# Kernel optimization log

Hardware: AMD Instinct MI355X
Metric: run time of the kernel (lower is better)

## Reference

```python
import jax, jax.numpy as jnp
import numpy as np

B, C, H, W = 8, 64, 256, 256   # input images
FH, FW = 64, 64                # low-res feature map
S = 256                        # superpixels per image (num[i] == S)


def setup_inputs() -> dict:
    key = jax.random.key(0)
    k1, k2, k3 = jax.random.split(key, 3)
    inp = jax.random.normal(k1, (B, C, H, W), dtype=jnp.float32)
    feat = jax.random.normal(k2, (B, C, FH, FW), dtype=jnp.float32)
    sp = jax.random.randint(k3, (B, 1, H, W), 0, S).astype(jnp.int64)
    num = jnp.full((B,), S, dtype=jnp.int64)
    return {"input": inp, "feature": feat, "sp": sp, "num": num}


def bilinear_align_corners(x, out_h, out_w):
    # F.interpolate(x, size, mode='bilinear', align_corners=True)
    _, _, in_h, in_w = x.shape
    ys = jnp.linspace(0.0, in_h - 1.0, out_h)
    xs = jnp.linspace(0.0, in_w - 1.0, out_w)
    y0 = jnp.floor(ys).astype(jnp.int32)
    x0 = jnp.floor(xs).astype(jnp.int32)
    y1 = jnp.minimum(y0 + 1, in_h - 1)
    x1 = jnp.minimum(x0 + 1, in_w - 1)
    wy = (ys - y0.astype(ys.dtype)).reshape(1, 1, out_h, 1)
    wx = (xs - x0.astype(xs.dtype)).reshape(1, 1, 1, out_w)
    rows = x[:, :, y0, :] * (1.0 - wy) + x[:, :, y1, :] * wy   # [B,C,out_h,in_w]
    return rows[:, :, :, x0] * (1.0 - wx) + rows[:, :, :, x1] * wx


def segment_scalar_means(x, sp, num):
    # torch: mean_values[i][j] = mean(x[i][sp[i]==j]) over channels AND pixels
    b = x.shape[0]
    px = x.mean(axis=1).reshape(b, -1)           # channel-mean per pixel [B, HW]
    ids = sp.reshape(b, -1)                      # [B, HW]
    seg_sum = jax.vmap(lambda v, i: jax.ops.segment_sum(v, i, num_segments=S))(px, ids)
    seg_cnt = jax.vmap(lambda i: jax.ops.segment_sum(jnp.ones(i.shape, jnp.float32), i, num_segments=S))(ids)
    m = jnp.where(seg_cnt > 0, seg_sum / jnp.maximum(seg_cnt, 1.0), 0.0)  # nan_to_num(0)
    valid = jnp.arange(S)[None, :] < num[:, None]                          # j < num[i]
    return jnp.where(valid, m, 0.0)              # [B, S]


def similarity_matrix(m):
    # mean_values broadcast to [B,S,C] => 1 - ||diff||/sqrt(C) == 1 - |m_j - m_k|
    return 1.0 - jnp.abs(m[:, :, None] - m[:, None, :])   # [B, S, S]


def reference(input, feature, sp, num):
    feat = bilinear_align_corners(feature, input.shape[-1], input.shape[-1])
    mat1 = similarity_matrix(segment_scalar_means(input, sp, num))
    mat2 = similarity_matrix(segment_scalar_means(feat, sp, num))
    return jnp.mean(jnp.abs(mat1 - mat2))   # nn.L1Loss()
```

## Files before the change

kernel.cpp:

```cpp
#include <hip/hip_runtime.h>

#define NB 8
#define NC 64
#define NH 256
#define NW 256
#define HW (NH*NW)
#define NFH 64
#define NFW 64
#define FHW (NFH*NFW)
#define NS 256
#define PPB 1024
#define NPB (HW/PPB)
#define NG 4
#define CPG (NC/NG)
#define NMAIN (NB*NPB*NG)
#define NRB (NB*NPB)

__global__ __launch_bounds__(256) void fmean_k(const float* __restrict__ feature,
                                               float* __restrict__ fmean) {
  __shared__ float4 s_p[8][32];
  const int b     = blockIdx.x >> 5;
  const int chunk = blockIdx.x & 31;
  const int q  = threadIdx.x & 31;
  const int cg = threadIdx.x >> 5;

  const float4* src = reinterpret_cast<const float4*>(
      feature + (size_t)(b * NC + cg * 8) * FHW) + chunk * 32 + q;
  float4 a = make_float4(0.f, 0.f, 0.f, 0.f);
  #pragma unroll
  for (int c = 0; c < 8; ++c) {
    float4 v = src[(size_t)c * (FHW / 4)];
    a.x += v.x; a.y += v.y; a.z += v.z; a.w += v.w;
  }
  s_p[cg][q] = a;
  __syncthreads();
  if (threadIdx.x < 32) {
    float4 r = make_float4(0.f, 0.f, 0.f, 0.f);
    #pragma unroll
    for (int g = 0; g < 8; ++g) {
      float4 v = s_p[g][threadIdx.x];
      r.x += v.x; r.y += v.y; r.z += v.z; r.w += v.w;
    }
    const float s = 1.0f / NC;
    r.x *= s; r.y *= s; r.z *= s; r.w *= s;
    reinterpret_cast<float4*>(fmean + (size_t)b * FHW)[chunk * 32 + threadIdx.x] = r;
  }
}

__global__ __launch_bounds__(256) void
main_k(const float* __restrict__ input,
       const int* __restrict__ sp,
       const float* __restrict__ fmean,
       float* __restrict__ part1,
       float* __restrict__ part2,
       float* __restrict__ partc,
       unsigned* __restrict__ counter) {
  __shared__ float s_f[FHW];
  __shared__ float s_bins[NS];
  __shared__ float s_fb[NS];
  __shared__ unsigned s_cnt[NS];

  const int bid = blockIdx.x;
  const int tid = threadIdx.x;
  if (bid == 0 && tid == 0) *counter = 0u;

  const int g  = bid & (NG - 1);
  const int pb = (bid >> 2) & (NPB - 1);
  const int b  = bid >> 8;
  const bool roleB = (g == 0);

  s_bins[tid] = 0.f;
  if (roleB) {
    const float4* fsrc = reinterpret_cast<const float4*>(fmean + (size_t)b * FHW);
    #pragma unroll
    for (int i = 0; i < 4; ++i)
      reinterpret_cast<float4*>(s_f)[tid + 256 * i] = fsrc[tid + 256 * i];
    s_fb[tid] = 0.f;
    s_cnt[tid] = 0u;
  }
  __syncthreads();

  const int p0 = pb * PPB + tid * 4;
  const float* ib = input + (size_t)(b * NC + g * CPG) * HW + p0;
  float4 acc = make_float4(0.f, 0.f, 0.f, 0.f);
  #pragma unroll 8
  for (int c = 0; c < CPG; ++c) {
    float4 v = *reinterpret_cast<const float4*>(ib + (size_t)c * HW);
    acc.x += v.x; acc.y += v.y; acc.z += v.z; acc.w += v.w;
  }
  const int4 idv = *reinterpret_cast<const int4*>(sp + (size_t)b * HW + p0);
  const float s = 1.0f / NC;
  atomicAdd(&s_bins[idv.x], acc.x * s);
  atomicAdd(&s_bins[idv.y], acc.y * s);
  atomicAdd(&s_bins[idv.z], acc.z * s);
  atomicAdd(&s_bins[idv.w], acc.w * s);

  if (roleB) {
    const int ids[4] = {idv.x, idv.y, idv.z, idv.w};
    const int h = p0 >> 8;
    const float yd = (float)h * (63.0f / 255.0f);
    const int y0 = (int)yd;
    const float wy = yd - (float)y0;
    const int y1 = min(y0 + 1, NFH - 1);
    const float* row0 = s_f + y0 * NFW;
    const float* row1 = s_f + y1 * NFW;
    #pragma unroll
    for (int i = 0; i < 4; ++i) {
      const int w = (p0 & 255) + i;
      const float xd = (float)w * (63.0f / 255.0f);
      const int x0 = (int)xd;
      const float wx = xd - (float)x0;
      const int x1 = min(x0 + 1, NFW - 1);
      float v0 = row0[x0] * (1.f - wy) + row1[x0] * wy;
      float v1 = row0[x1] * (1.f - wy) + row1[x1] * wy;
      float fv = v0 * (1.f - wx) + v1 * wx;
      atomicAdd(&s_fb[ids[i]], fv);
      atomicAdd(&s_cnt[ids[i]], 1u);
    }
  }
  __syncthreads();

  part1[(size_t)bid * NS + tid] = s_bins[tid];
  if (roleB) {
    const int r = (b << 6) | pb;
    part2[(size_t)r * NS + tid] = s_fb[tid];
    partc[(size_t)r * NS + tid] = (float)s_cnt[tid];
  }
}

__global__ __launch_bounds__(256) void
finalize_k(const float* __restrict__ part1,
           const float* __restrict__ part2,
           const float* __restrict__ partc,
           const int* __restrict__ num,
           float* __restrict__ partial,
           unsigned* __restrict__ counter,
           float* __restrict__ out) {
  __shared__ float m1[NS];
  __shared__ float m2[NS];
  __shared__ float red[256];
  const int b = blockIdx.x;
  const int j = threadIdx.x;

  float s1 = 0.f;
  const float* p1 = part1 + (size_t)b * 256 * NS + j;
  #pragma unroll 8
  for (int t = 0; t < 256; ++t) s1 += p1[(size_t)t * NS];

  float s2 = 0.f, c = 0.f;
  const float* p2 = part2 + (size_t)b * 64 * NS + j;
  const float* pc = partc + (size_t)b * 64 * NS + j;
  #pragma unroll 8
  for (int t = 0; t < 64; ++t) { s2 += p2[(size_t)t * NS]; c += pc[(size_t)t * NS]; }

  const int nb = num[b];
  float v1 = 0.f, v2 = 0.f;
  if (j < nb && c > 0.f) {
    float invc = 1.0f / c;
    v1 = s1 * invc;
    v2 = s2 * invc;
  }
  m1[j] = v1; m2[j] = v2;
  __syncthreads();

  float accum = 0.f;
  #pragma unroll 8
  for (int k = 0; k < NS; ++k) {
    accum += fabsf(fabsf(v1 - m1[k]) - fabsf(v2 - m2[k]));
  }
  red[j] = accum;
  __syncthreads();
  for (int st = 128; st > 0; st >>= 1) {
    if (j < st) red[j] += red[j + st];
    __syncthreads();
  }

  if (j == 0) {
    atomicExch(&partial[b], red[0]);
    __threadfence();
    unsigned old = atomicAdd(counter, 1u);
    if (old == NB - 1) {
      __threadfence();
      float sAll = 0.f;
      #pragma unroll
      for (int i = 0; i < NB; ++i) sAll += atomicAdd(&partial[i], 0.0f);
      out[0] = sAll / (float)(NB * NS * NS);
      *counter = 0u;
    }
  }
}

extern "C" void kernel_launch(void* const* d_in, const int* in_sizes, int n_in,
                              void* d_out, int out_size, void* d_ws, size_t ws_size,
                              hipStream_t stream) {
  const float* input   = (const float*)d_in[0];
  const float* feature = (const float*)d_in[1];
  const int*   sp      = (const int*)d_in[2];
  const int*   num     = (const int*)d_in[3];
  float* out = (float*)d_out;

  float* ws      = (float*)d_ws;
  float*    part1   = ws;
  float*    part2   = part1 + (size_t)NMAIN * NS;
  float*    partc   = part2 + (size_t)NRB * NS;
  float*    fmean   = partc + (size_t)NRB * NS;
  float*    partial = fmean + NB * FHW;
  unsigned* counter = (unsigned*)(partial + 8);

  fmean_k<<<NB * 32, 256, 0, stream>>>(feature, fmean);
  main_k<<<NMAIN, 256, 0, stream>>>(input, sp, fmean, part1, part2, partc, counter);
  finalize_k<<<NB, 256, 0, stream>>>(part1, part2, partc, num, partial, counter, out);
}
```

Baseline: 63.02 us.

## Split feature-bilinear work into separate blocks and drop 16KB shared fmean tile

The bilinear/count work no longer runs inside one of every four input-reduction blocks. It now goes to 512 extra dedicated blocks that read the feature mean directly from global memory instead of staging a 16KB shared tile. This removes the per-block shared-memory footprint and the load imbalance between role-B and regular blocks, which should raise occupancy for the bandwidth-bound input reduction. Input loads also switch to nontemporal vector loads. The cost is that sp is now read twice for the role-B pixels and the fmean reads become uncached gathers from global memory.

```diff
diff --git a/kernel.cpp b/kernel.cpp
--- a/kernel.cpp
+++ b/kernel.cpp
@@ -16,6 +16,8 @@
 #define NMAIN (NB*NPB*NG)
 #define NRB (NB*NPB)
 
+typedef float f32x4 __attribute__((ext_vector_type(4)));
+
 __global__ __launch_bounds__(256) void fmean_k(const float* __restrict__ feature,
                                                float* __restrict__ fmean) {
   __shared__ float4 s_p[8][32];
@@ -55,7 +57,6 @@
        float* __restrict__ part2,
        float* __restrict__ partc,
        unsigned* __restrict__ counter) {
-  __shared__ float s_f[FHW];
   __shared__ float s_bins[NS];
   __shared__ float s_fb[NS];
   __shared__ unsigned s_cnt[NS];
@@ -64,46 +65,54 @@
   const int tid = threadIdx.x;
   if (bid == 0 && tid == 0) *counter = 0u;
 
-  const int g  = bid & (NG - 1);
-  const int pb = (bid >> 2) & (NPB - 1);
-  const int b  = bid >> 8;
-  const bool roleB = (g == 0);
-
-  s_bins[tid] = 0.f;
-  if (roleB) {
-    const float4* fsrc = reinterpret_cast<const float4*>(fmean + (size_t)b * FHW);
+  if (bid < NMAIN) {
+    const int g  = bid & (NG - 1);
+    const int pb = (bid >> 2) & (NPB - 1);
+    const int b  = bid >> 8;
+
+    s_bins[tid] = 0.f;
+    __syncthreads();
+
+    const int p0 = pb * PPB + tid * 4;
+    const float* ib = input + (size_t)(b * NC + g * CPG) * HW + p0;
+    f32x4 acc = (f32x4)(0.f);
     #pragma unroll
-    for (int i = 0; i < 4; ++i)
-      reinterpret_cast<float4*>(s_f)[tid + 256 * i] = fsrc[tid + 256 * i];
+    for (int c = 0; c < CPG; ++c) {
+      f32x4 v = __builtin_nontemporal_load(
+          reinterpret_cast<const f32x4*>(ib + (size_t)c * HW));
+      acc += v;
+    }
+    const int4 idv = *reinterpret_cast<const int4*>(sp + (size_t)b * HW + p0);
+    const float s = 1.0f / NC;
+    atomicAdd(&s_bins[idv.x], acc.x * s);
+    atomicAdd(&s_bins[idv.y], acc.y * s);
+    atomicAdd(&s_bins[idv.z], acc.z * s);
+    atomicAdd(&s_bins[idv.w], acc.w * s);
+    __syncthreads();
+
+    part1[(size_t)bid * NS + tid] = s_bins[tid];
+  } else {
+    const int r  = bid - NMAIN;
+    const int b  = r >> 6;
+    const int pb = r & (NPB - 1);
+
     s_fb[tid] = 0.f;
     s_cnt[tid] = 0u;
-  }
-  __syncthreads();
-
-  const int p0 = pb * PPB + tid * 4;
-  const float* ib = input + (size_t)(b * NC + g * CPG) * HW + p0;
-  float4 acc = make_float4(0.f, 0.f, 0.f, 0.f);
-  #pragma unroll 8
-  for (int c = 0; c < CPG; ++c) {
-    float4 v = *reinterpret_cast<const float4*>(ib + (size_t)c * HW);
-    acc.x += v.x; acc.y += v.y; acc.z += v.z; acc.w += v.w;
-  }
-  const int4 idv = *reinterpret_cast<const int4*>(sp + (size_t)b * HW + p0);
-  const float s = 1.0f / NC;
-  atomicAdd(&s_bins[idv.x], acc.x * s);
-  atomicAdd(&s_bins[idv.y], acc.y * s);
-  atomicAdd(&s_bins[idv.z], acc.z * s);
-  atomicAdd(&s_bins[idv.w], acc.w * s);
-
-  if (roleB) {
+    __syncthreads();
+
+    const int p0 = pb * PPB + tid * 4;
+    const int4 idv = *reinterpret_cast<const int4*>(sp + (size_t)b * HW + p0);
     const int ids[4] = {idv.x, idv.y, idv.z, idv.w};
+
+    const float* fm = fmean + (size_t)b * FHW;
     const int h = p0 >> 8;
     const float yd = (float)h * (63.0f / 255.0f);
     const int y0 = (int)yd;
     const float wy = yd - (float)y0;
     const int y1 = min(y0 + 1, NFH - 1);
-    const float* row0 = s_f + y0 * NFW;
-    const float* row1 = s_f + y1 * NFW;
+    const float* row0 = fm + y0 * NFW;
+    const float* row1 = fm + y1 * NFW;
+
     #pragma unroll
     for (int i = 0; i < 4; ++i) {
       const int w = (p0 & 255) + i;
@@ -117,12 +126,8 @@
       atomicAdd(&s_fb[ids[i]], fv);
       atomicAdd(&s_cnt[ids[i]], 1u);
     }
-  }
-  __syncthreads();
-
-  part1[(size_t)bid * NS + tid] = s_bins[tid];
-  if (roleB) {
-    const int r = (b << 6) | pb;
+    __syncthreads();
+
     part2[(size_t)r * NS + tid] = s_fb[tid];
     partc[(size_t)r * NS + tid] = (float)s_cnt[tid];
   }
@@ -208,6 +213,6 @@
   unsigned* counter = (unsigned*)(partial + 8);
 
   fmean_k<<<NB * 32, 256, 0, stream>>>(feature, fmean);
-  main_k<<<NMAIN, 256, 0, stream>>>(input, sp, fmean, part1, part2, partc, counter);
+  main_k<<<NMAIN + NRB, 256, 0, stream>>>(input, sp, fmean, part1, part2, partc, counter);
   finalize_k<<<NB, 256, 0, stream>>>(part1, part2, partc, num, partial, counter, out);
 }
```

Result: faster. 58.27 us (-7.5%).
